# Kernel optimization log

Hardware: AMD Instinct MI355X
Metric: run time of the kernel (lower is better)

## Reference

```python
import jax, jax.numpy as jnp
import numpy as np

E, K, H, I, T = 32, 4, 1024, 1024, 1024
ALPHA, BETA = 1.702, 1.0  # swiglu_alpha, swiglu_beta from the module


def setup_inputs() -> dict:
    key = jax.random.key(0)
    k0, k1, k2, k3 = jax.random.split(key, 4)
    return {
        "hidden_states": jax.random.normal(k0, (T, H), jnp.float32),
        "gate_w": jax.random.normal(k1, (H, E), jnp.float32) * (H ** -0.5),
        "gate_b": jnp.zeros((E,), jnp.float32),
        # pair_wise_act=True: gate/up are interleaved along the last dim of w1's output
        "w1": jax.random.normal(k2, (E, H, 2 * I), jnp.float32) * (H ** -0.5),
        "b1": jnp.zeros((E, 2 * I), jnp.float32),
        "w2": jax.random.normal(k3, (E, I, H), jnp.float32) * (I ** -0.5),
        "b2": jnp.zeros((E, H), jnp.float32),
    }


def reference(hidden_states, gate_w, gate_b, w1, b1, w2, b2):
    # Router gate (ReplicatedLinear with bias)
    router_logits = hidden_states @ gate_w + gate_b            # [T, E]
    probs = jax.nn.softmax(router_logits, axis=-1)
    topk_w, topk_idx = jax.lax.top_k(probs, K)                 # [T, K]
    # renormalize (norm_topk_prob=True)
    topk_w = topk_w / jnp.sum(topk_w, axis=-1, keepdims=True)
    # combine weights per (expert, token): sum over slots where idx == e
    onehot = (topk_idx[None, :, :] == jnp.arange(E)[:, None, None])  # [E, T, K]
    combine_w = jnp.sum(onehot * topk_w[None, :, :], axis=-1)        # [E, T]
    # Expert MLPs (grouped GEMM expressed as dense-per-expert einsum)
    h = jnp.einsum('th,ehd->etd', hidden_states, w1) + b1[:, None, :]  # [E, T, 2I]
    gate = h[..., 0::2]   # interleaved pairwise gate
    up = h[..., 1::2]     # interleaved pairwise up
    act = (up + BETA) * gate * jax.nn.sigmoid(ALPHA * gate)           # [E, T, I]
    y = jnp.einsum('eti,eih->eth', act, w2) + b2[:, None, :]          # [E, T, H]
    # weighted combine across selected experts
    return jnp.einsum('eth,et->th', y, combine_w)                     # [T, H]
```

## Files before the change

kernel.cpp:

```cpp
#include <hip/hip_runtime.h>
#include <hip/hip_bf16.h>
#include <math.h>

#define E_ 32
#define K_ 4
#define H_ 1024
#define I_ 1024
#define T_ 1024
#define TWO_I 2048

typedef __attribute__((ext_vector_type(4))) float float4v;
typedef __attribute__((ext_vector_type(8))) short short8v;
typedef __attribute__((ext_vector_type(4))) short short4v;

__device__ __forceinline__ unsigned short f2bf(float f) {
    unsigned u = __float_as_uint(f);
    u = (u + 0x7FFFu + ((u >> 16) & 1u)) >> 16;
    return (unsigned short)u;
}
__device__ __forceinline__ short4v cvt4(float4v v) {
    short4v r;
    r[0] = (short)f2bf(v[0]); r[1] = (short)f2bf(v[1]);
    r[2] = (short)f2bf(v[2]); r[3] = (short)f2bf(v[3]);
    return r;
}
__device__ __forceinline__ int permpos(int k4) {
    return ((k4 >> 5) << 5) + (((k4 >> 2) & 3) << 3) + (((k4 >> 4) & 1) << 2);
}

__global__ __launch_bounds__(256) void router_kernel(
    const float* __restrict__ hs, const float* __restrict__ gw,
    const float* __restrict__ gb, int* __restrict__ counts,
    int* __restrict__ token_list, float* __restrict__ weight_list) {
    int wv = threadIdx.x >> 6, lane = threadIdx.x & 63;
    int t = blockIdx.x * 4 + wv;
    int e = lane & 31;
    int half = lane >> 5;
    const float* hrow = hs + (size_t)t * H_;
    const float* gcol = gw + e;
    float a0 = 0.f, a1 = 0.f;
    int hb = half * 512;
#pragma unroll 4
    for (int h = 0; h < 512; h += 2) {
        a0 = fmaf(hrow[hb + h],     gcol[(size_t)(hb + h) * E_], a0);
        a1 = fmaf(hrow[hb + h + 1], gcol[(size_t)(hb + h + 1) * E_], a1);
    }
    float part = a0 + a1;
    part += __shfl_xor(part, 32);
    float cur = part + gb[e];

    int idx4[K_]; float val4[K_];
#pragma unroll
    for (int k = 0; k < K_; ++k) {
        float m = cur;
#pragma unroll
        for (int d = 1; d < 64; d <<= 1) m = fmaxf(m, __shfl_xor(m, d));
        unsigned long long b = __ballot(cur == m);
        int l = __ffsll(b) - 1;
        idx4[k] = l & 31; val4[k] = m;
        if (e == (l & 31)) cur = -INFINITY;
    }
    float mx = val4[0], s = 0.f, wv4[K_];
#pragma unroll
    for (int k = 0; k < K_; ++k) { wv4[k] = expf(val4[k] - mx); s += wv4[k]; }
    float inv = 1.f / s;
    if (lane < K_) {
        int ex = idx4[lane];
        int slot = atomicAdd(&counts[ex], 1);
        token_list[ex * T_ + slot] = t;
        weight_list[ex * T_ + slot] = wv4[lane] * inv;
    }
}

__global__ void scan_kernel(const int* __restrict__ counts, int* __restrict__ offsets) {
    if (threadIdx.x == 0) {
        int o = 0;
        for (int e = 0; e < E_; ++e) { offsets[e] = o; o += counts[e]; }
        offsets[E_] = o;
    }
}

__global__ void compact_kernel(const int* __restrict__ counts,
                               const int* __restrict__ offsets,
                               const int* __restrict__ token_list,
                               const float* __restrict__ weight_list,
                               int* __restrict__ tok_of_slot,
                               float* __restrict__ w_of_slot) {
    int e = blockIdx.x;
    int cnt = counts[e];
    int off = offsets[e];
    for (int s = threadIdx.x; s < cnt; s += blockDim.x) {
        tok_of_slot[off + s] = token_list[e * T_ + s];
        w_of_slot[off + s]   = weight_list[e * T_ + s];
    }
}

__global__ __launch_bounds__(256, 2) void gemm1_kernel(
    const float* __restrict__ hs, const float* __restrict__ w1,
    const float* __restrict__ b1, const int* __restrict__ counts,
    const int* __restrict__ offsets, const int* __restrict__ tok_of_slot,
    unsigned short* __restrict__ actb) {
    int e = blockIdx.z;
    int cnt = counts[e];
    int m0 = blockIdx.y * 128;
    if (m0 >= cnt) return;
    int cb = blockIdx.x * 128;
    int off = offsets[e];
    const float* w1e = w1 + (size_t)e * H_ * TWO_I;

    __shared__ __align__(16) short As[128 * 64];
    __shared__ __align__(16) short Bs[8192];

    int tid = threadIdx.x;
    int lane = tid & 63;
    int wid = tid >> 6;
    int wm = wid >> 1, wn = wid & 1;
    int g = lane >> 4;
    int l15 = lane & 15;
    unsigned baddr = (unsigned)(size_t)(&Bs[0]) + (unsigned)(lane * 8) + (unsigned)(wn * 8192);

    int k4 = (tid & 15) << 2;
    const float* aptr[8]; int awidx[8];
#pragma unroll
    for (int i = 0; i < 8; ++i) {
        int row = i * 16 + (tid >> 4);
        int gr = m0 + row;
        aptr[i] = (gr < cnt) ? hs + (size_t)tok_of_slot[off + gr] * H_ + k4 : nullptr;
        awidx[i] = row * 64 + (permpos(k4) ^ ((row & 7) << 3));
    }
    int n4 = (tid & 31) << 2;
    const float* bptr[8]; int bwidx[8];
#pragma unroll
    for (int i = 0; i < 8; ++i) {
        int krow = i * 8 + (tid >> 5);
        bptr[i] = w1e + (size_t)krow * TWO_I + cb + n4;
        bwidx[i] = ((n4 >> 4) * 16 + (krow >> 2)) * 64 + (krow & 3) * 16 + (n4 & 15);
    }

    float4v acc[4][4];
#pragma unroll
    for (int i = 0; i < 4; ++i)
#pragma unroll
        for (int j = 0; j < 4; ++j) acc[i][j] = (float4v){0.f, 0.f, 0.f, 0.f};

    float4v ra[8], rb[8];
    const float4v z4 = {0.f, 0.f, 0.f, 0.f};
#pragma unroll
    for (int i = 0; i < 8; ++i) ra[i] = aptr[i] ? *(const float4v*)(aptr[i]) : z4;
#pragma unroll
    for (int i = 0; i < 8; ++i) rb[i] = *(const float4v*)(bptr[i]);

#pragma unroll 1
    for (int k0 = 0; k0 < H_; k0 += 64) {
#pragma unroll
        for (int i = 0; i < 8; ++i) *(short4v*)&As[awidx[i]] = cvt4(ra[i]);
#pragma unroll
        for (int i = 0; i < 8; ++i) *(short4v*)&Bs[bwidx[i]] = cvt4(rb[i]);
        __syncthreads();
        if (k0 + 64 < H_) {
            int kn = k0 + 64;
#pragma unroll
            for (int i = 0; i < 8; ++i) ra[i] = aptr[i] ? *(const float4v*)(aptr[i] + kn) : z4;
#pragma unroll
            for (int i = 0; i < 8; ++i) rb[i] = *(const float4v*)(bptr[i] + (size_t)kn * TWO_I);
        }
        __builtin_amdgcn_sched_barrier(0);
#pragma unroll
        for (int s = 0; s < 2; ++s) {
            short8v a[4];
#pragma unroll
            for (int mi = 0; mi < 4; ++mi) {
                int row = wm * 64 + mi * 16 + l15;
                a[mi] = *(const short8v*)&As[row * 64 + ((s * 32 + g * 8) ^ ((row & 7) << 3))];
            }
            short4v bl[4], bh[4];
#pragma unroll
            for (int ni = 0; ni < 4; ++ni) {
                unsigned ad = baddr + (unsigned)(ni * 2048 + s * 1024);
                asm volatile("ds_read_b64_tr_b16 %0, %1" : "=v"(bl[ni]) : "v"(ad));
                asm volatile("ds_read_b64_tr_b16 %0, %1" : "=v"(bh[ni]) : "v"(ad + 512u));
            }
            asm volatile("s_waitcnt lgkmcnt(0)" ::: "memory");
            __builtin_amdgcn_sched_barrier(0);
#pragma unroll
            for (int ni = 0; ni < 4; ++ni) {
                short8v b;
                b[0] = bl[ni][0]; b[1] = bl[ni][1]; b[2] = bl[ni][2]; b[3] = bl[ni][3];
                b[4] = bh[ni][0]; b[5] = bh[ni][1]; b[6] = bh[ni][2]; b[7] = bh[ni][3];
#pragma unroll
                for (int mi = 0; mi < 4; ++mi)
                    acc[mi][ni] = __builtin_amdgcn_mfma_f32_16x16x32_bf16(a[mi], b, acc[mi][ni], 0, 0, 0);
            }
        }
        __syncthreads();
    }
    const float* b1e = b1 + (size_t)e * TWO_I;
#pragma unroll
    for (int mi = 0; mi < 4; ++mi) {
#pragma unroll
        for (int r = 0; r < 4; ++r) {
            int gm = m0 + wm * 64 + mi * 16 + g * 4 + r;
#pragma unroll
            for (int ni = 0; ni < 4; ++ni) {
                float v = acc[mi][ni][r];
                float o = __shfl_xor(v, 1);
                if (!(lane & 1) && gm < cnt) {
                    int wc = cb + wn * 64 + ni * 16 + l15;
                    float gate = v + b1e[wc];
                    float up   = o + b1e[wc + 1];
                    float sg = 1.f / (1.f + __expf(-1.702f * gate));
                    float av = (up + 1.f) * gate * sg;
                    actb[(size_t)(off + gm) * I_ + (wc >> 1)] = f2bf(av);
                }
            }
        }
    }
}

__global__ __launch_bounds__(256, 2) void gemm2_kernel(
    const unsigned short* __restrict__ actb, const float* __restrict__ w2,
    const float* __restrict__ b2, const int* __restrict__ counts,
    const int* __restrict__ offsets, const int* __restrict__ tok_of_slot,
    const float* __restrict__ w_of_slot, float* __restrict__ out) {
    int e = blockIdx.z;
    int cnt = counts[e];
    int m0 = blockIdx.y * 128;
    if (m0 >= cnt) return;
    int h0 = (blockIdx.x >> 1) * 128;
    int kbase = (blockIdx.x & 1) * 512;
    int off = offsets[e];
    const float* w2e = w2 + (size_t)e * I_ * H_;

    __shared__ __align__(16) short As[128 * 64];
    __shared__ __align__(16) short Bs[8192];

    int tid = threadIdx.x;
    int lane = tid & 63;
    int wid = tid >> 6;
    int wm = wid >> 1, wn = wid & 1;
    int g = lane >> 4;
    int l15 = lane & 15;
    unsigned baddr = (unsigned)(size_t)(&Bs[0]) + (unsigned)(lane * 8) + (unsigned)(wn * 8192);

    int q = tid & 7;
    const unsigned short* aptr[4]; int aw0[4], aw1[4];
#pragma unroll
    for (int i = 0; i < 4; ++i) {
        int row = i * 32 + (tid >> 3);
        int gr = m0 + row;
        aptr[i] = (gr < cnt) ? actb + (size_t)(off + gr) * I_ + kbase + q * 8 : nullptr;
        int sw = (row & 7) << 3;
        aw0[i] = row * 64 + (permpos(q * 8) ^ sw);
        aw1[i] = row * 64 + (permpos(q * 8 + 4) ^ sw);
    }
    int n4 = (tid & 31) << 2;
    const float* bptr[8]; int bwidx[8];
#pragma unroll
    for (int i = 0; i < 8; ++i) {
        int krow = i * 8 + (tid >> 5);
        bptr[i] = w2e + (size_t)(kbase + krow) * H_ + h0 + n4;
        bwidx[i] = ((n4 >> 4) * 16 + (krow >> 2)) * 64 + (krow & 3) * 16 + (n4 & 15);
    }

    float4v acc[4][4];
#pragma unroll
    for (int i = 0; i < 4; ++i)
#pragma unroll
        for (int j = 0; j < 4; ++j) acc[i][j] = (float4v){0.f, 0.f, 0.f, 0.f};

    short8v ra[4]; float4v rb[8];
    const short8v z8 = {0, 0, 0, 0, 0, 0, 0, 0};
#pragma unroll
    for (int i = 0; i < 4; ++i) ra[i] = aptr[i] ? *(const short8v*)(aptr[i]) : z8;
#pragma unroll
    for (int i = 0; i < 8; ++i) rb[i] = *(const float4v*)(bptr[i]);

#pragma unroll 1
    for (int k0 = 0; k0 < 512; k0 += 64) {
#pragma unroll
        for (int i = 0; i < 4; ++i) {
            short8v v = ra[i];
            short4v lo, hi;
            lo[0] = v[0]; lo[1] = v[1]; lo[2] = v[2]; lo[3] = v[3];
            hi[0] = v[4]; hi[1] = v[5]; hi[2] = v[6]; hi[3] = v[7];
            *(short4v*)&As[aw0[i]] = lo;
            *(short4v*)&As[aw1[i]] = hi;
        }
#pragma unroll
        for (int i = 0; i < 8; ++i) *(short4v*)&Bs[bwidx[i]] = cvt4(rb[i]);
        __syncthreads();
        if (k0 + 64 < 512) {
            int kn = k0 + 64;
#pragma unroll
            for (int i = 0; i < 4; ++i) ra[i] = aptr[i] ? *(const short8v*)(aptr[i] + kn) : z8;
#pragma unroll
            for (int i = 0; i < 8; ++i) rb[i] = *(const float4v*)(bptr[i] + (size_t)kn * H_);
        }
        __builtin_amdgcn_sched_barrier(0);
#pragma unroll
        for (int s = 0; s < 2; ++s) {
            short8v a[4];
#pragma unroll
            for (int mi = 0; mi < 4; ++mi) {
                int row = wm * 64 + mi * 16 + l15;
                a[mi] = *(const short8v*)&As[row * 64 + ((s * 32 + g * 8) ^ ((row & 7) << 3))];
            }
            short4v bl[4], bh[4];
#pragma unroll
            for (int ni = 0; ni < 4; ++ni) {
                unsigned ad = baddr + (unsigned)(ni * 2048 + s * 1024);
                asm volatile("ds_read_b64_tr_b16 %0, %1" : "=v"(bl[ni]) : "v"(ad));
                asm volatile("ds_read_b64_tr_b16 %0, %1" : "=v"(bh[ni]) : "v"(ad + 512u));
            }
            asm volatile("s_waitcnt lgkmcnt(0)" ::: "memory");
            __builtin_amdgcn_sched_barrier(0);
#pragma unroll
            for (int ni = 0; ni < 4; ++ni) {
                short8v b;
                b[0] = bl[ni][0]; b[1] = bl[ni][1]; b[2] = bl[ni][2]; b[3] = bl[ni][3];
                b[4] = bh[ni][0]; b[5] = bh[ni][1]; b[6] = bh[ni][2]; b[7] = bh[ni][3];
#pragma unroll
                for (int mi = 0; mi < 4; ++mi)
                    acc[mi][ni] = __builtin_amdgcn_mfma_f32_16x16x32_bf16(a[mi], b, acc[mi][ni], 0, 0, 0);
            }
        }
        __syncthreads();
    }
    const float* b2e = b2 + (size_t)e * H_;
    bool addbias = (kbase == 0);
#pragma unroll
    for (int mi = 0; mi < 4; ++mi) {
#pragma unroll
        for (int r = 0; r < 4; ++r) {
            int gm = m0 + wm * 64 + mi * 16 + g * 4 + r;
            if (gm < cnt) {
                int gl = off + gm;
                int t = tok_of_slot[gl];
                float wgt = w_of_slot[gl];
#pragma unroll
                for (int ni = 0; ni < 4; ++ni) {
                    int h = h0 + wn * 64 + ni * 16 + l15;
                    float v = acc[mi][ni][r];
                    if (addbias) v += b2e[h];
                    atomicAdd(&out[(size_t)t * H_ + h], v * wgt);
                }
            }
        }
    }
}

extern "C" void kernel_launch(void* const* d_in, const int* in_sizes, int n_in,
                              void* d_out, int out_size, void* d_ws, size_t ws_size,
                              hipStream_t stream) {
    const float* hs = (const float*)d_in[0];
    const float* gw = (const float*)d_in[1];
    const float* gb = (const float*)d_in[2];
    const float* w1 = (const float*)d_in[3];
    const float* b1 = (const float*)d_in[4];
    const float* w2 = (const float*)d_in[5];
    const float* b2 = (const float*)d_in[6];
    float* out = (float*)d_out;

    char* ws = (char*)d_ws;
    int*   counts      = (int*)ws;
    int*   offsets     = (int*)(ws + 128);
    int*   tok_of_slot = (int*)(ws + 512);
    float* w_of_slot   = (float*)(ws + 512 + 16384);
    int*   token_list  = (int*)(ws + 512 + 32768);
    float* weight_list = (float*)(ws + 512 + 32768 + 131072);
    unsigned short* actb = (unsigned short*)(ws + (1 << 20));

    hipMemsetAsync(counts, 0, 32 * sizeof(int), stream);
    hipMemsetAsync(d_out, 0, (size_t)out_size * sizeof(float), stream);

    router_kernel<<<T_ / 4, 256, 0, stream>>>(hs, gw, gb, counts, token_list, weight_list);
    scan_kernel<<<1, 64, 0, stream>>>(counts, offsets);
    compact_kernel<<<E_, 256, 0, stream>>>(counts, offsets, token_list, weight_list,
                                           tok_of_slot, w_of_slot);
    gemm1_kernel<<<dim3(TWO_I / 128, T_ / 128, E_), 256, 0, stream>>>(
        hs, w1, b1, counts, offsets, tok_of_slot, actb);
    gemm2_kernel<<<dim3((H_ / 128) * 2, T_ / 128, E_), 256, 0, stream>>>(
        actb, w2, b2, counts, offsets, tok_of_slot, w_of_slot, out);
}
```

Baseline: 250.9 us.

## Double-buffer LDS in expert GEMMs, halve N tile, drop scan/compact kernels

```diff
diff --git a/kernel.cpp b/kernel.cpp
--- a/kernel.cpp
+++ b/kernel.cpp
@@ -72,44 +72,70 @@
     }
 }
 
-__global__ void scan_kernel(const int* __restrict__ counts, int* __restrict__ offsets) {
-    if (threadIdx.x == 0) {
-        int o = 0;
-        for (int e = 0; e < E_; ++e) { offsets[e] = o; o += counts[e]; }
-        offsets[E_] = o;
-    }
-}
-
-__global__ void compact_kernel(const int* __restrict__ counts,
-                               const int* __restrict__ offsets,
-                               const int* __restrict__ token_list,
-                               const float* __restrict__ weight_list,
-                               int* __restrict__ tok_of_slot,
-                               float* __restrict__ w_of_slot) {
-    int e = blockIdx.x;
-    int cnt = counts[e];
-    int off = offsets[e];
-    for (int s = threadIdx.x; s < cnt; s += blockDim.x) {
-        tok_of_slot[off + s] = token_list[e * T_ + s];
-        w_of_slot[off + s]   = weight_list[e * T_ + s];
-    }
-}
-
-__global__ __launch_bounds__(256, 2) void gemm1_kernel(
+#define G1_COMPUTE(BUF)                                                        \
+    _Pragma("unroll")                                                          \
+    for (int s = 0; s < 2; ++s) {                                              \
+        short8v afr[4];                                                        \
+        _Pragma("unroll")                                                      \
+        for (int mi = 0; mi < 4; ++mi) {                                       \
+            int row = wm * 64 + mi * 16 + l15;                                 \
+            afr[mi] = *(const short8v*)&As[BUF][row * 64 + ((s * 32 + g * 8) ^ sw)]; \
+        }                                                                      \
+        short4v bl[2], bh[2];                                                  \
+        _Pragma("unroll")                                                      \
+        for (int ni = 0; ni < 2; ++ni) {                                       \
+            unsigned ad = ((BUF) ? trb1 : trb0) + (unsigned)(ni * 2048 + s * 1024); \
+            asm volatile("ds_read_b64_tr_b16 %0, %1" : "=v"(bl[ni]) : "v"(ad));     \
+            asm volatile("ds_read_b64_tr_b16 %0, %1" : "=v"(bh[ni]) : "v"(ad + 512u)); \
+        }                                                                      \
+        asm volatile("s_waitcnt lgkmcnt(0)" ::: "memory");                     \
+        __builtin_amdgcn_sched_barrier(0);                                     \
+        _Pragma("unroll")                                                      \
+        for (int ni = 0; ni < 2; ++ni) {                                       \
+            short8v b;                                                         \
+            b[0] = bl[ni][0]; b[1] = bl[ni][1]; b[2] = bl[ni][2]; b[3] = bl[ni][3]; \
+            b[4] = bh[ni][0]; b[5] = bh[ni][1]; b[6] = bh[ni][2]; b[7] = bh[ni][3]; \
+            _Pragma("unroll")                                                  \
+            for (int mi = 0; mi < 4; ++mi)                                     \
+                acc[mi][ni] = __builtin_amdgcn_mfma_f32_16x16x32_bf16(afr[mi], b, acc[mi][ni], 0, 0, 0); \
+        }                                                                      \
+    }
+
+#define G1_STEP(BUF, KN, ISLAST)                                               \
+    {                                                                          \
+        __syncthreads();                                                       \
+        if (!(ISLAST)) {                                                       \
+            _Pragma("unroll")                                                  \
+            for (int i = 0; i < 8; ++i)                                        \
+                ra[i] = aptr[i] ? *(const float4v*)(aptr[i] + (KN)) : z4;      \
+            _Pragma("unroll")                                                  \
+            for (int i = 0; i < 4; ++i)                                        \
+                rb[i] = *(const float4v*)(bptrB + (size_t)(KN)*TWO_I + (size_t)(i * 16) * TWO_I); \
+        }                                                                      \
+        __builtin_amdgcn_sched_barrier(0);                                     \
+        G1_COMPUTE(BUF)                                                        \
+        if (!(ISLAST)) {                                                       \
+            _Pragma("unroll")                                                  \
+            for (int i = 0; i < 8; ++i) *(short4v*)&As[(BUF) ^ 1][awidx[i]] = cvt4(ra[i]); \
+            _Pragma("unroll")                                                  \
+            for (int i = 0; i < 4; ++i) *(short4v*)&Bs[(BUF) ^ 1][bwidx[i]] = cvt4(rb[i]); \
+        }                                                                      \
+    }
+
+__global__ __launch_bounds__(256, 3) void gemm1_kernel(
     const float* __restrict__ hs, const float* __restrict__ w1,
     const float* __restrict__ b1, const int* __restrict__ counts,
-    const int* __restrict__ offsets, const int* __restrict__ tok_of_slot,
-    unsigned short* __restrict__ actb) {
+    const int* __restrict__ token_list, unsigned short* __restrict__ actb) {
     int e = blockIdx.z;
     int cnt = counts[e];
     int m0 = blockIdx.y * 128;
     if (m0 >= cnt) return;
-    int cb = blockIdx.x * 128;
-    int off = offsets[e];
+    int cb = blockIdx.x * 64;
     const float* w1e = w1 + (size_t)e * H_ * TWO_I;
-
-    __shared__ __align__(16) short As[128 * 64];
-    __shared__ __align__(16) short Bs[8192];
+    const int* tl = token_list + e * T_;
+
+    __shared__ __align__(16) short As[2][128 * 64];
+    __shared__ __align__(16) short Bs[2][64 * 64];
 
     int tid = threadIdx.x;
     int lane = tid & 63;
@@ -117,7 +143,9 @@
     int wm = wid >> 1, wn = wid & 1;
     int g = lane >> 4;
     int l15 = lane & 15;
-    unsigned baddr = (unsigned)(size_t)(&Bs[0]) + (unsigned)(lane * 8) + (unsigned)(wn * 8192);
+    int sw = (l15 & 7) << 3;
+    unsigned trb0 = (unsigned)(size_t)(&Bs[0][0]) + (unsigned)(lane * 8) + (unsigned)(wn * 4096);
+    unsigned trb1 = (unsigned)(size_t)(&Bs[1][0]) + (unsigned)(lane * 8) + (unsigned)(wn * 4096);
 
     int k4 = (tid & 15) << 2;
     const float* aptr[8]; int awidx[8];
@@ -125,75 +153,40 @@
     for (int i = 0; i < 8; ++i) {
         int row = i * 16 + (tid >> 4);
         int gr = m0 + row;
-        aptr[i] = (gr < cnt) ? hs + (size_t)tok_of_slot[off + gr] * H_ + k4 : nullptr;
+        aptr[i] = (gr < cnt) ? hs + (size_t)tl[gr] * H_ + k4 : nullptr;
         awidx[i] = row * 64 + (permpos(k4) ^ ((row & 7) << 3));
     }
-    int n4 = (tid & 31) << 2;
-    const float* bptr[8]; int bwidx[8];
-#pragma unroll
-    for (int i = 0; i < 8; ++i) {
-        int krow = i * 8 + (tid >> 5);
-        bptr[i] = w1e + (size_t)krow * TWO_I + cb + n4;
-        bwidx[i] = ((n4 >> 4) * 16 + (krow >> 2)) * 64 + (krow & 3) * 16 + (n4 & 15);
-    }
-
-    float4v acc[4][4];
+    const float* bptrB = w1e + (size_t)(tid >> 4) * TWO_I + cb + k4;
+    int bwidx[4];
+#pragma unroll
+    for (int i = 0; i < 4; ++i) {
+        int krow = i * 16 + (tid >> 4);
+        bwidx[i] = ((k4 >> 4) * 16 + (krow >> 2)) * 64 + (krow & 3) * 16 + (k4 & 15);
+    }
+
+    float4v acc[4][2];
 #pragma unroll
     for (int i = 0; i < 4; ++i)
 #pragma unroll
-        for (int j = 0; j < 4; ++j) acc[i][j] = (float4v){0.f, 0.f, 0.f, 0.f};
-
-    float4v ra[8], rb[8];
+        for (int j = 0; j < 2; ++j) acc[i][j] = (float4v){0.f, 0.f, 0.f, 0.f};
+
+    float4v ra[8], rb[4];
     const float4v z4 = {0.f, 0.f, 0.f, 0.f};
 #pragma unroll
     for (int i = 0; i < 8; ++i) ra[i] = aptr[i] ? *(const float4v*)(aptr[i]) : z4;
 #pragma unroll
-    for (int i = 0; i < 8; ++i) rb[i] = *(const float4v*)(bptr[i]);
+    for (int i = 0; i < 4; ++i) rb[i] = *(const float4v*)(bptrB + (size_t)(i * 16) * TWO_I);
+#pragma unroll
+    for (int i = 0; i < 8; ++i) *(short4v*)&As[0][awidx[i]] = cvt4(ra[i]);
+#pragma unroll
+    for (int i = 0; i < 4; ++i) *(short4v*)&Bs[0][bwidx[i]] = cvt4(rb[i]);
 
 #pragma unroll 1
-    for (int k0 = 0; k0 < H_; k0 += 64) {
-#pragma unroll
-        for (int i = 0; i < 8; ++i) *(short4v*)&As[awidx[i]] = cvt4(ra[i]);
-#pragma unroll
-        for (int i = 0; i < 8; ++i) *(short4v*)&Bs[bwidx[i]] = cvt4(rb[i]);
-        __syncthreads();
-        if (k0 + 64 < H_) {
-            int kn = k0 + 64;
-#pragma unroll
-            for (int i = 0; i < 8; ++i) ra[i] = aptr[i] ? *(const float4v*)(aptr[i] + kn) : z4;
-#pragma unroll
-            for (int i = 0; i < 8; ++i) rb[i] = *(const float4v*)(bptr[i] + (size_t)kn * TWO_I);
-        }
-        __builtin_amdgcn_sched_barrier(0);
-#pragma unroll
-        for (int s = 0; s < 2; ++s) {
-            short8v a[4];
-#pragma unroll
-            for (int mi = 0; mi < 4; ++mi) {
-                int row = wm * 64 + mi * 16 + l15;
-                a[mi] = *(const short8v*)&As[row * 64 + ((s * 32 + g * 8) ^ ((row & 7) << 3))];
-            }
-            short4v bl[4], bh[4];
-#pragma unroll
-            for (int ni = 0; ni < 4; ++ni) {
-                unsigned ad = baddr + (unsigned)(ni * 2048 + s * 1024);
-                asm volatile("ds_read_b64_tr_b16 %0, %1" : "=v"(bl[ni]) : "v"(ad));
-                asm volatile("ds_read_b64_tr_b16 %0, %1" : "=v"(bh[ni]) : "v"(ad + 512u));
-            }
-            asm volatile("s_waitcnt lgkmcnt(0)" ::: "memory");
-            __builtin_amdgcn_sched_barrier(0);
-#pragma unroll
-            for (int ni = 0; ni < 4; ++ni) {
-                short8v b;
-                b[0] = bl[ni][0]; b[1] = bl[ni][1]; b[2] = bl[ni][2]; b[3] = bl[ni][3];
-                b[4] = bh[ni][0]; b[5] = bh[ni][1]; b[6] = bh[ni][2]; b[7] = bh[ni][3];
-#pragma unroll
-                for (int mi = 0; mi < 4; ++mi)
-                    acc[mi][ni] = __builtin_amdgcn_mfma_f32_16x16x32_bf16(a[mi], b, acc[mi][ni], 0, 0, 0);
-            }
-        }
-        __syncthreads();
-    }
+    for (int kk = 0; kk < H_; kk += 128) {
+        G1_STEP(0, kk + 64, false)
+        G1_STEP(1, kk + 128, (kk + 128) >= H_)
+    }
+
     const float* b1e = b1 + (size_t)e * TWO_I;
 #pragma unroll
     for (int mi = 0; mi < 4; ++mi) {
@@ -201,38 +194,66 @@
         for (int r = 0; r < 4; ++r) {
             int gm = m0 + wm * 64 + mi * 16 + g * 4 + r;
 #pragma unroll
-            for (int ni = 0; ni < 4; ++ni) {
+            for (int ni = 0; ni < 2; ++ni) {
                 float v = acc[mi][ni][r];
                 float o = __shfl_xor(v, 1);
                 if (!(lane & 1) && gm < cnt) {
-                    int wc = cb + wn * 64 + ni * 16 + l15;
+                    int wc = cb + wn * 32 + ni * 16 + l15;
                     float gate = v + b1e[wc];
                     float up   = o + b1e[wc + 1];
                     float sg = 1.f / (1.f + __expf(-1.702f * gate));
                     float av = (up + 1.f) * gate * sg;
-                    actb[(size_t)(off + gm) * I_ + (wc >> 1)] = f2bf(av);
+                    actb[(size_t)(e * T_ + gm) * I_ + (wc >> 1)] = f2bf(av);
                 }
             }
         }
     }
 }
 
-__global__ __launch_bounds__(256, 2) void gemm2_kernel(
+#define G2_STEP(BUF, KN, ISLAST)                                               \
+    {                                                                          \
+        __syncthreads();                                                       \
+        if (!(ISLAST)) {                                                       \
+            _Pragma("unroll")                                                  \
+            for (int i = 0; i < 4; ++i)                                        \
+                ra2[i] = aptr[i] ? *(const short8v*)(aptr[i] + (KN)) : z8;     \
+            _Pragma("unroll")                                                  \
+            for (int i = 0; i < 4; ++i)                                        \
+                rb[i] = *(const float4v*)(bptrB + (size_t)(KN)*H_ + (size_t)(i * 16) * H_); \
+        }                                                                      \
+        __builtin_amdgcn_sched_barrier(0);                                     \
+        G1_COMPUTE(BUF)                                                        \
+        if (!(ISLAST)) {                                                       \
+            _Pragma("unroll")                                                  \
+            for (int i = 0; i < 4; ++i) {                                      \
+                short8v v = ra2[i];                                            \
+                short4v lo, hi;                                                \
+                lo[0] = v[0]; lo[1] = v[1]; lo[2] = v[2]; lo[3] = v[3];        \
+                hi[0] = v[4]; hi[1] = v[5]; hi[2] = v[6]; hi[3] = v[7];        \
+                *(short4v*)&As[(BUF) ^ 1][aw0[i]] = lo;                        \
+                *(short4v*)&As[(BUF) ^ 1][aw1[i]] = hi;                        \
+            }                                                                  \
+            _Pragma("unroll")                                                  \
+            for (int i = 0; i < 4; ++i) *(short4v*)&Bs[(BUF) ^ 1][bwidx[i]] = cvt4(rb[i]); \
+        }                                                                      \
+    }
+
+__global__ __launch_bounds__(256, 3) void gemm2_kernel(
     const unsigned short* __restrict__ actb, const float* __restrict__ w2,
     const float* __restrict__ b2, const int* __restrict__ counts,
-    const int* __restrict__ offsets, const int* __restrict__ tok_of_slot,
-    const float* __restrict__ w_of_slot, float* __restrict__ out) {
+    const int* __restrict__ token_list, const float* __restrict__ weight_list,
+    float* __restrict__ out) {
     int e = blockIdx.z;
     int cnt = counts[e];
     int m0 = blockIdx.y * 128;
     if (m0 >= cnt) return;
-    int h0 = (blockIdx.x >> 1) * 128;
+    int h0 = (blockIdx.x >> 1) * 64;
     int kbase = (blockIdx.x & 1) * 512;
-    int off = offsets[e];
     const float* w2e = w2 + (size_t)e * I_ * H_;
-
-    __shared__ __align__(16) short As[128 * 64];
-    __shared__ __align__(16) short Bs[8192];
+    const int* tl = token_list + e * T_;
+
+    __shared__ __align__(16) short As[2][128 * 64];
+    __shared__ __align__(16) short Bs[2][64 * 64];
 
     int tid = threadIdx.x;
     int lane = tid & 63;
@@ -240,7 +261,9 @@
     int wm = wid >> 1, wn = wid & 1;
     int g = lane >> 4;
     int l15 = lane & 15;
-    unsigned baddr = (unsigned)(size_t)(&Bs[0]) + (unsigned)(lane * 8) + (unsigned)(wn * 8192);
+    int sw = (l15 & 7) << 3;
+    unsigned trb0 = (unsigned)(size_t)(&Bs[0][0]) + (unsigned)(lane * 8) + (unsigned)(wn * 4096);
+    unsigned trb1 = (unsigned)(size_t)(&Bs[1][0]) + (unsigned)(lane * 8) + (unsigned)(wn * 4096);
 
     int q = tid & 7;
     const unsigned short* aptr[4]; int aw0[4], aw1[4];
@@ -248,85 +271,52 @@
     for (int i = 0; i < 4; ++i) {
         int row = i * 32 + (tid >> 3);
         int gr = m0 + row;
-        aptr[i] = (gr < cnt) ? actb + (size_t)(off + gr) * I_ + kbase + q * 8 : nullptr;
-        int sw = (row & 7) << 3;
-        aw0[i] = row * 64 + (permpos(q * 8) ^ sw);
-        aw1[i] = row * 64 + (permpos(q * 8 + 4) ^ sw);
-    }
-    int n4 = (tid & 31) << 2;
-    const float* bptr[8]; int bwidx[8];
-#pragma unroll
-    for (int i = 0; i < 8; ++i) {
-        int krow = i * 8 + (tid >> 5);
-        bptr[i] = w2e + (size_t)(kbase + krow) * H_ + h0 + n4;
-        bwidx[i] = ((n4 >> 4) * 16 + (krow >> 2)) * 64 + (krow & 3) * 16 + (n4 & 15);
-    }
-
-    float4v acc[4][4];
+        aptr[i] = (gr < cnt) ? actb + (size_t)(e * T_ + gr) * I_ + kbase + q * 8 : nullptr;
+        int swr = (row & 7) << 3;
+        aw0[i] = row * 64 + (permpos(q * 8) ^ swr);
+        aw1[i] = row * 64 + (permpos(q * 8 + 4) ^ swr);
+    }
+    int k4 = (tid & 15) << 2;
+    const float* bptrB = w2e + (size_t)(kbase + (tid >> 4)) * H_ + h0 + k4;
+    int bwidx[4];
+#pragma unroll
+    for (int i = 0; i < 4; ++i) {
+        int krow = i * 16 + (tid >> 4);
+        bwidx[i] = ((k4 >> 4) * 16 + (krow >> 2)) * 64 + (krow & 3) * 16 + (k4 & 15);
+    }
+
+    float4v acc[4][2];
 #pragma unroll
     for (int i = 0; i < 4; ++i)
 #pragma unroll
-        for (int j = 0; j < 4; ++j) acc[i][j] = (float4v){0.f, 0.f, 0.f, 0.f};
-
-    short8v ra[4]; float4v rb[8];
+        for (int j = 0; j < 2; ++j) acc[i][j] = (float4v){0.f, 0.f, 0.f, 0.f};
+
+    short8v ra2[4]; float4v rb[4];
     const short8v z8 = {0, 0, 0, 0, 0, 0, 0, 0};
 #pragma unroll
-    for (int i = 0; i < 4; ++i) ra[i] = aptr[i] ? *(const short8v*)(aptr[i]) : z8;
-#pragma unroll
-    for (int i = 0; i < 8; ++i) rb[i] = *(const float4v*)(bptr[i]);
+    for (int i = 0; i < 4; ++i) ra2[i] = aptr[i] ? *(const short8v*)(aptr[i]) : z8;
+#pragma unroll
+    for (int i = 0; i < 4; ++i) rb[i] = *(const float4v*)(bptrB + (size_t)(i * 16) * H_);
+#pragma unroll
+    for (int i = 0; i < 4; ++i) {
+        short8v v = ra2[i];
+        short4v lo, hi;
+        lo[0] = v[0]; lo[1] = v[1]; lo[2] = v[2]; lo[3] = v[3];
+        hi[0] = v[4]; hi[1] = v[5]; hi[2] = v[6]; hi[3] = v[7];
+        *(short4v*)&As[0][aw0[i]] = lo;
+        *(short4v*)&As[0][aw1[i]] = hi;
+    }
+#pragma unroll
+    for (int i = 0; i < 4; ++i) *(short4v*)&Bs[0][bwidx[i]] = cvt4(rb[i]);
 
 #pragma unroll 1
-    for (int k0 = 0; k0 < 512; k0 += 64) {
-#pragma unroll
-        for (int i = 0; i < 4; ++i) {
-            short8v v = ra[i];
-            short4v lo, hi;
-            lo[0] = v[0]; lo[1] = v[1]; lo[2] = v[2]; lo[3] = v[3];
-            hi[0] = v[4]; hi[1] = v[5]; hi[2] = v[6]; hi[3] = v[7];
-            *(short4v*)&As[aw0[i]] = lo;
-            *(short4v*)&As[aw1[i]] = hi;
-        }
-#pragma unroll
-        for (int i = 0; i < 8; ++i) *(short4v*)&Bs[bwidx[i]] = cvt4(rb[i]);
-        __syncthreads();
-        if (k0 + 64 < 512) {
-            int kn = k0 + 64;
-#pragma unroll
-            for (int i = 0; i < 4; ++i) ra[i] = aptr[i] ? *(const short8v*)(aptr[i] + kn) : z8;
-#pragma unroll
-            for (int i = 0; i < 8; ++i) rb[i] = *(const float4v*)(bptr[i] + (size_t)kn * H_);
-        }
-        __builtin_amdgcn_sched_barrier(0);
-#pragma unroll
-        for (int s = 0; s < 2; ++s) {
-            short8v a[4];
-#pragma unroll
-            for (int mi = 0; mi < 4; ++mi) {
-                int row = wm * 64 + mi * 16 + l15;
-                a[mi] = *(const short8v*)&As[row * 64 + ((s * 32 + g * 8) ^ ((row & 7) << 3))];
-            }
-            short4v bl[4], bh[4];
-#pragma unroll
-            for (int ni = 0; ni < 4; ++ni) {
-                unsigned ad = baddr + (unsigned)(ni * 2048 + s * 1024);
-                asm volatile("ds_read_b64_tr_b16 %0, %1" : "=v"(bl[ni]) : "v"(ad));
-                asm volatile("ds_read_b64_tr_b16 %0, %1" : "=v"(bh[ni]) : "v"(ad + 512u));
-            }
-            asm volatile("s_waitcnt lgkmcnt(0)" ::: "memory");
-            __builtin_amdgcn_sched_barrier(0);
-#pragma unroll
-            for (int ni = 0; ni < 4; ++ni) {
-                short8v b;
-                b[0] = bl[ni][0]; b[1] = bl[ni][1]; b[2] = bl[ni][2]; b[3] = bl[ni][3];
-                b[4] = bh[ni][0]; b[5] = bh[ni][1]; b[6] = bh[ni][2]; b[7] = bh[ni][3];
-#pragma unroll
-                for (int mi = 0; mi < 4; ++mi)
-                    acc[mi][ni] = __builtin_amdgcn_mfma_f32_16x16x32_bf16(a[mi], b, acc[mi][ni], 0, 0, 0);
-            }
-        }
-        __syncthreads();
-    }
+    for (int kk = 0; kk < 512; kk += 128) {
+        G2_STEP(0, kk + 64, false)
+        G2_STEP(1, kk + 128, (kk + 128) >= 512)
+    }
+
     const float* b2e = b2 + (size_t)e * H_;
+    const float* wl = weight_list + e * T_;
     bool addbias = (kbase == 0);
 #pragma unroll
     for (int mi = 0; mi < 4; ++mi) {
@@ -334,12 +324,11 @@
         for (int r = 0; r < 4; ++r) {
             int gm = m0 + wm * 64 + mi * 16 + g * 4 + r;
             if (gm < cnt) {
-                int gl = off + gm;
-                int t = tok_of_slot[gl];
-                float wgt = w_of_slot[gl];
-#pragma unroll
-                for (int ni = 0; ni < 4; ++ni) {
-                    int h = h0 + wn * 64 + ni * 16 + l15;
+                int t = tl[gm];
+                float wgt = wl[gm];
+#pragma unroll
+                for (int ni = 0; ni < 2; ++ni) {
+                    int h = h0 + wn * 32 + ni * 16 + l15;
                     float v = acc[mi][ni][r];
                     if (addbias) v += b2e[h];
                     atomicAdd(&out[(size_t)t * H_ + h], v * wgt);
@@ -363,22 +352,16 @@
 
     char* ws = (char*)d_ws;
     int*   counts      = (int*)ws;
-    int*   offsets     = (int*)(ws + 128);
-    int*   tok_of_slot = (int*)(ws + 512);
-    float* w_of_slot   = (float*)(ws + 512 + 16384);
-    int*   token_list  = (int*)(ws + 512 + 32768);
-    float* weight_list = (float*)(ws + 512 + 32768 + 131072);
+    int*   token_list  = (int*)(ws + 4096);
+    float* weight_list = (float*)(ws + 4096 + 131072);
     unsigned short* actb = (unsigned short*)(ws + (1 << 20));
 
     hipMemsetAsync(counts, 0, 32 * sizeof(int), stream);
     hipMemsetAsync(d_out, 0, (size_t)out_size * sizeof(float), stream);
 
     router_kernel<<<T_ / 4, 256, 0, stream>>>(hs, gw, gb, counts, token_list, weight_list);
-    scan_kernel<<<1, 64, 0, stream>>>(counts, offsets);
-    compact_kernel<<<E_, 256, 0, stream>>>(counts, offsets, token_list, weight_list,
-                                           tok_of_slot, w_of_slot);
-    gemm1_kernel<<<dim3(TWO_I / 128, T_ / 128, E_), 256, 0, stream>>>(
-        hs, w1, b1, counts, offsets, tok_of_slot, actb);
-    gemm2_kernel<<<dim3((H_ / 128) * 2, T_ / 128, E_), 256, 0, stream>>>(
-        actb, w2, b2, counts, offsets, tok_of_slot, w_of_slot, out);
-}
+    gemm1_kernel<<<dim3(TWO_I / 64, T_ / 128, E_), 256, 0, stream>>>(
+        hs, w1, b1, counts, token_list, actb);
+    gemm2_kernel<<<dim3((H_ / 64) * 2, T_ / 128, E_), 256, 0, stream>>>(
+        actb, w2, b2, counts, token_list, weight_list, out);
+}
```

New measurement: 214.8 us. -14.4%, faster.
